# Kernel tuning notes

Measured on AMD Instinct MI355X. Metric: run time of the kernel, lower is better.

The kernel has to match this reference:

```python
import jax, jax.numpy as jnp
import numpy as np

NUM_EXPERTS = 64
TOP_K = 8
TEMPERATURE = 1.0


def setup_inputs() -> dict:
    key = jax.random.key(0)
    k1, k2 = jax.random.split(key)
    B, D, E = 32768, 2048, NUM_EXPERTS
    r = jax.random.normal(k1, (B, D), dtype=jnp.float32)
    W = jax.random.normal(k2, (E, D), dtype=jnp.float32) * (1.0 / np.sqrt(D))
    b = jnp.zeros((E,), dtype=jnp.float32)
    return {"r": r, "W": W, "b": b}


def reference(r, W, b):
    # logits: (B, E) = r @ W^T + b, then temperature scaling
    logits = (jnp.einsum('bd,ed->be', r, W) + b) / TEMPERATURE
    weights_soft = jax.nn.softmax(logits, axis=-1)
    if TOP_K is not None and TOP_K < NUM_EXPERTS:
        topk_vals, topk_idx = jax.lax.top_k(weights_soft, TOP_K)
        mask = jnp.zeros_like(weights_soft)
        mask = jax.vmap(lambda m, i: m.at[i].set(1.0))(mask, topk_idx)
        weights_hard = weights_soft * mask
        weights_hard = weights_hard / (weights_hard.sum(axis=-1, keepdims=True) + 1e-9)
    else:
        weights_hard = weights_soft
    return (weights_hard, weights_soft)
```

## Files before the change

kernel.cpp:

```cpp
#include <hip/hip_runtime.h>
#include <hip/hip_bf16.h>
#include <stdint.h>


#define D_DIM 2048
#define E_DIM 64
#define B_DIM 32768
#define TOPK 8
#define NK 16

typedef __bf16 bf16x8 __attribute__((ext_vector_type(8)));
typedef float f32x4 __attribute__((ext_vector_type(4)));

__global__ __launch_bounds__(256) void w_prep(const float* __restrict__ W,
                                              __bf16* __restrict__ P) {
    const int K = blockIdx.x;
    const int u = threadIdx.x;
    const float* src = W + (size_t)(u >> 2) * D_DIM + K * 32 + (u & 3) * 8;
    __bf16* dst = P + (size_t)K * 6144 + u * 8;
    bf16x8 o1, o2, o3;
    #pragma unroll
    for (int j = 0; j < 8; ++j) {
        float x  = src[j];
        __bf16 h1 = (__bf16)x;
        float r1 = x - (float)h1;
        __bf16 h2 = (__bf16)r1;
        float r2 = r1 - (float)h2;
        o1[j] = h1; o2[j] = h2; o3[j] = (__bf16)r2;
    }
    *(bf16x8*)(dst)        = o1;
    *(bf16x8*)(dst + 2048) = o2;
    *(bf16x8*)(dst + 4096) = o3;
}

__global__ __launch_bounds__(256, 4) void moe_gate(const float* __restrict__ r,
                                                   const __bf16* __restrict__ P,
                                                   const float* __restrict__ bias,
                                                   float* __restrict__ out) {
    __shared__ float lg[4][16][E_DIM + 1];

    const int t    = threadIdx.x;
    const int wv   = t >> 6;
    const int lane = t & 63;
    const int lrow = lane & 15;
    const int quad = lane >> 4;
    const int row0 = blockIdx.x * 16;

    const __bf16* Pq = P + (size_t)wv * NK * 6144 + quad * 8 + lrow * 32;
    const float* ra = r + (size_t)(row0 + lrow) * D_DIM + wv * 512 + quad * 8;

    f32x4 accM[4] = {};
    f32x4 accD[4] = {};
    f32x4 accL[4] = {};

    float4 a0 = *(const float4*)(ra);
    float4 a1 = *(const float4*)(ra + 4);

    #pragma unroll 2
    for (int ks = 0; ks < NK; ++ks) {
        const int kn = ks + 1;
        float4 na0 = a0, na1 = a1;
        if (kn < NK) {
            na0 = *(const float4*)(ra + kn * 32);
            na1 = *(const float4*)(ra + kn * 32 + 4);
        }

        const __bf16* bb = Pq + (size_t)ks * 6144;
        bf16x8 B[3][4];
        #pragma unroll
        for (int s = 0; s < 3; ++s)
            #pragma unroll
            for (int n = 0; n < 4; ++n)
                B[s][n] = *(const bf16x8*)(bb + s * 2048 + n * 512);

        float av[8] = {a0.x, a0.y, a0.z, a0.w, a1.x, a1.y, a1.z, a1.w};
        bf16x8 A1, A2, A3;
        #pragma unroll
        for (int j = 0; j < 8; ++j) {
            float x  = av[j];
            __bf16 h1 = (__bf16)x;
            float r1 = x - (float)h1;
            __bf16 h2 = (__bf16)r1;
            float r2 = r1 - (float)h2;
            A1[j] = h1; A2[j] = h2; A3[j] = (__bf16)r2;
        }

        #pragma unroll
        for (int n = 0; n < 4; ++n) {
            accM[n] = __builtin_amdgcn_mfma_f32_16x16x32_bf16(A1, B[0][n], accM[n], 0, 0, 0);
            accD[n] = __builtin_amdgcn_mfma_f32_16x16x32_bf16(A1, B[1][n], accD[n], 0, 0, 0);
            accD[n] = __builtin_amdgcn_mfma_f32_16x16x32_bf16(A2, B[0][n], accD[n], 0, 0, 0);
            accL[n] = __builtin_amdgcn_mfma_f32_16x16x32_bf16(A1, B[2][n], accL[n], 0, 0, 0);
            accL[n] = __builtin_amdgcn_mfma_f32_16x16x32_bf16(A2, B[1][n], accL[n], 0, 0, 0);
            accL[n] = __builtin_amdgcn_mfma_f32_16x16x32_bf16(A3, B[0][n], accL[n], 0, 0, 0);
        }

        a0 = na0; a1 = na1;
    }

    #pragma unroll
    for (int n = 0; n < 4; ++n) {
        int col = n * 16 + lrow;
        #pragma unroll
        for (int i = 0; i < 4; ++i)
            lg[wv][quad * 4 + i][col] = accM[n][i] + (accD[n][i] + accL[n][i]);
    }
    __syncthreads();

    const float bcol = bias[lane];
    for (int rr = wv; rr < 16; rr += 4) {
        float logit = ((lg[0][rr][lane] + lg[1][rr][lane]) +
                       (lg[2][rr][lane] + lg[3][rr][lane])) + bcol;
        float mx = logit;
        #pragma unroll
        for (int s = 32; s >= 1; s >>= 1) mx = fmaxf(mx, __shfl_xor(mx, s));
        float ex = expf(logit - mx);
        float sm = ex;
        #pragma unroll
        for (int s = 32; s >= 1; s >>= 1) sm += __shfl_xor(sm, s);
        float soft = ex / sm;

        bool  sel    = false;
        float topsum = 0.0f;
        #pragma unroll
        for (int it = 0; it < TOPK; ++it) {
            float cand = sel ? -1.0f : soft;
            float cm = cand;
            #pragma unroll
            for (int s = 32; s >= 1; s >>= 1) cm = fmaxf(cm, __shfl_xor(cm, s));
            unsigned long long ball = __ballot(cand == cm);
            int leader = __ffsll(ball) - 1;
            if (lane == leader) sel = true;
            topsum += cm;
        }
        float hard = sel ? soft / (topsum + 1e-9f) : 0.0f;

        size_t orow = (size_t)(row0 + rr) * E_DIM + lane;
        out[orow] = hard;
        out[(size_t)B_DIM * E_DIM + orow] = soft;
    }
}

extern "C" void kernel_launch(void* const* d_in, const int* in_sizes, int n_in,
                              void* d_out, int out_size, void* d_ws, size_t ws_size,
                              hipStream_t stream) {
    const float* r = (const float*)d_in[0];
    const float* W = (const float*)d_in[1];
    const float* b = (const float*)d_in[2];
    float* out = (float*)d_out;
    __bf16* P = (__bf16*)d_ws;

    w_prep<<<64, 256, 0, stream>>>(W, P);
    moe_gate<<<2048, 256, 0, stream>>>(r, P, b, out);
}
```

Baseline: 442.4 us.

## Double-buffer W and activation register loads two k-steps ahead

Restructures the main loop into a two-stage register pipeline. Both the bf16 weight fragments and the fp32 activations for step k+2 are loaded while step k is being computed, and the loop is fully unrolled. Previously only the activations were prefetched and the weights were loaded right before use. The wider prefetch is meant to hide global load latency. It roughly doubles register use for the weights, so the launch-bounds occupancy hint is relaxed from 4 to 2 blocks per CU, which cuts the number of resident waves available for latency hiding.

```diff
diff --git a/kernel.cpp b/kernel.cpp
--- a/kernel.cpp
+++ b/kernel.cpp
@@ -33,7 +33,7 @@
     *(bf16x8*)(dst + 4096) = o3;
 }
 
-__global__ __launch_bounds__(256, 4) void moe_gate(const float* __restrict__ r,
+__global__ __launch_bounds__(256, 2) void moe_gate(const float* __restrict__ r,
                                                    const __bf16* __restrict__ P,
                                                    const float* __restrict__ bias,
                                                    float* __restrict__ out) {
@@ -53,50 +53,65 @@
     f32x4 accD[4] = {};
     f32x4 accL[4] = {};
 
-    float4 a0 = *(const float4*)(ra);
-    float4 a1 = *(const float4*)(ra + 4);
+    bf16x8 B0[3][4], B1[3][4];
+    float4 p00, p01, p10, p11;
 
-    #pragma unroll 2
-    for (int ks = 0; ks < NK; ++ks) {
-        const int kn = ks + 1;
-        float4 na0 = a0, na1 = a1;
-        if (kn < NK) {
-            na0 = *(const float4*)(ra + kn * 32);
-            na1 = *(const float4*)(ra + kn * 32 + 4);
-        }
+#define LOADB(Bd, kk) do {                                                  \
+        const __bf16* bb_ = Pq + (size_t)(kk) * 6144;                       \
+        _Pragma("unroll")                                                   \
+        for (int s_ = 0; s_ < 3; ++s_)                                      \
+            _Pragma("unroll")                                               \
+            for (int n_ = 0; n_ < 4; ++n_)                                  \
+                Bd[s_][n_] = *(const bf16x8*)(bb_ + s_ * 2048 + n_ * 512);  \
+    } while (0)
 
-        const __bf16* bb = Pq + (size_t)ks * 6144;
-        bf16x8 B[3][4];
-        #pragma unroll
-        for (int s = 0; s < 3; ++s)
-            #pragma unroll
-            for (int n = 0; n < 4; ++n)
-                B[s][n] = *(const bf16x8*)(bb + s * 2048 + n * 512);
+#define LOADA(pa_, pb_, kk) do {                                            \
+        pa_ = *(const float4*)(ra + (kk) * 32);                             \
+        pb_ = *(const float4*)(ra + (kk) * 32 + 4);                         \
+    } while (0)
 
-        float av[8] = {a0.x, a0.y, a0.z, a0.w, a1.x, a1.y, a1.z, a1.w};
-        bf16x8 A1, A2, A3;
-        #pragma unroll
-        for (int j = 0; j < 8; ++j) {
-            float x  = av[j];
-            __bf16 h1 = (__bf16)x;
-            float r1 = x - (float)h1;
-            __bf16 h2 = (__bf16)r1;
-            float r2 = r1 - (float)h2;
-            A1[j] = h1; A2[j] = h2; A3[j] = (__bf16)r2;
-        }
+#define COMPUTE(Bd, pa_, pb_) do {                                          \
+        float av_[8] = {pa_.x, pa_.y, pa_.z, pa_.w,                         \
+                        pb_.x, pb_.y, pb_.z, pb_.w};                        \
+        bf16x8 A1_, A2_, A3_;                                               \
+        _Pragma("unroll")                                                   \
+        for (int j_ = 0; j_ < 8; ++j_) {                                    \
+            float x_  = av_[j_];                                            \
+            __bf16 h1_ = (__bf16)x_;                                        \
+            float r1_ = x_ - (float)h1_;                                    \
+            __bf16 h2_ = (__bf16)r1_;                                       \
+            float r2_ = r1_ - (float)h2_;                                   \
+            A1_[j_] = h1_; A2_[j_] = h2_; A3_[j_] = (__bf16)r2_;            \
+        }                                                                   \
+        _Pragma("unroll")                                                   \
+        for (int n_ = 0; n_ < 4; ++n_) {                                    \
+            accM[n_] = __builtin_amdgcn_mfma_f32_16x16x32_bf16(A1_, Bd[0][n_], accM[n_], 0, 0, 0); \
+            accD[n_] = __builtin_amdgcn_mfma_f32_16x16x32_bf16(A1_, Bd[1][n_], accD[n_], 0, 0, 0); \
+            accD[n_] = __builtin_amdgcn_mfma_f32_16x16x32_bf16(A2_, Bd[0][n_], accD[n_], 0, 0, 0); \
+            accL[n_] = __builtin_amdgcn_mfma_f32_16x16x32_bf16(A1_, Bd[2][n_], accL[n_], 0, 0, 0); \
+            accL[n_] = __builtin_amdgcn_mfma_f32_16x16x32_bf16(A2_, Bd[1][n_], accL[n_], 0, 0, 0); \
+            accL[n_] = __builtin_amdgcn_mfma_f32_16x16x32_bf16(A3_, Bd[0][n_], accL[n_], 0, 0, 0); \
+        }                                                                   \
+    } while (0)
 
-        #pragma unroll
-        for (int n = 0; n < 4; ++n) {
-            accM[n] = __builtin_amdgcn_mfma_f32_16x16x32_bf16(A1, B[0][n], accM[n], 0, 0, 0);
-            accD[n] = __builtin_amdgcn_mfma_f32_16x16x32_bf16(A1, B[1][n], accD[n], 0, 0, 0);
-            accD[n] = __builtin_amdgcn_mfma_f32_16x16x32_bf16(A2, B[0][n], accD[n], 0, 0, 0);
-            accL[n] = __builtin_amdgcn_mfma_f32_16x16x32_bf16(A1, B[2][n], accL[n], 0, 0, 0);
-            accL[n] = __builtin_amdgcn_mfma_f32_16x16x32_bf16(A2, B[1][n], accL[n], 0, 0, 0);
-            accL[n] = __builtin_amdgcn_mfma_f32_16x16x32_bf16(A3, B[0][n], accL[n], 0, 0, 0);
-        }
+    LOADB(B0, 0); LOADA(p00, p01, 0);
+    LOADB(B1, 1); LOADA(p10, p11, 1);
 
-        a0 = na0; a1 = na1;
+    #pragma unroll
+    for (int ks = 0; ks < NK; ks += 2) {
+        const int k2 = (ks + 2 < NK) ? ks + 2 : ks;
+        const int k3 = (ks + 3 < NK) ? ks + 3 : ks + 1;
+
+        COMPUTE(B0, p00, p01);
+        LOADB(B0, k2); LOADA(p00, p01, k2);
+
+        COMPUTE(B1, p10, p11);
+        LOADB(B1, k3); LOADA(p10, p11, k3);
     }
+
+#undef LOADB
+#undef LOADA
+#undef COMPUTE
 
     #pragma unroll
     for (int n = 0; n < 4; ++n) {
```

After: 457.5 us. 3.4% more time.
